# Optimization experiments

Measured on AMD Instinct MI355X. Metric: run time of the kernel, lower is better.

The kernel has to match this reference:

```python
import jax, jax.numpy as jnp
import numpy as np

G, H, D = 8, 16, 64           # groups, heads-per-group, head_size
B, S = 2, 1024                # sequences, tokens per sequence (T = B*S packed)
HID = G * H * D               # 8192
SCALE = D ** -0.5


def _rotary(x, cos, sin):
    # NeoX-style rotary. x: [T, nh, D]; cos/sin: [T, D//2]
    half = D // 2
    c = cos[:, None, :]
    s = sin[:, None, :]
    x1, x2 = x[..., :half], x[..., half:]
    return jnp.concatenate([x1 * c - x2 * s, x2 * c + x1 * s], axis=-1)


def setup_inputs() -> dict:
    key = jax.random.key(0)
    ks = jax.random.split(key, 6)
    T = B * S
    hidden_states = jax.random.normal(ks[0], (T, HID), jnp.float32)
    # true rotary tables from positions (base 10000)
    pos = jnp.tile(jnp.arange(S, dtype=jnp.float32), B)            # [T]
    inv_freq = 1.0 / (10000.0 ** (jnp.arange(0, D, 2, dtype=jnp.float32) / D))
    freqs = pos[:, None] * inv_freq[None, :]                       # [T, D//2]
    cos, sin = jnp.cos(freqs), jnp.sin(freqs)
    w_qkv = jax.random.normal(ks[1], (HID, G * (H + 2) * D), jnp.float32) * (HID ** -0.5)
    b_qkv = jax.random.normal(ks[2], (G * (H + 2) * D,), jnp.float32) * 0.02
    w_dense = jax.random.normal(ks[3], (G * H * D, HID), jnp.float32) * (HID ** -0.5)
    b_dense = jax.random.normal(ks[4], (HID,), jnp.float32) * 0.02
    kv_cache = jnp.zeros((2, 4096, G, D), jnp.float32)
    slots = jnp.arange(T, dtype=jnp.int32)
    return dict(hidden_states=hidden_states, cos=cos, sin=sin,
                w_qkv=w_qkv, b_qkv=b_qkv, w_dense=w_dense, b_dense=b_dense,
                kv_cache=kv_cache, slots=slots, batch_size=B)


def reference(hidden_states, cos, sin, w_qkv, b_qkv, w_dense, b_dense,
              kv_cache, slots, batch_size):
    T = hidden_states.shape[0]
    qkv = hidden_states @ w_qkv + b_qkv                    # [T, G*(H+2)*D]
    qkv = qkv.reshape(T, G, H + 2, D)
    query = qkv[:, :, :H, :].reshape(T, G * H, D)          # [T, G*H, D]
    k = qkv[:, :, H, :]                                    # [T, G, D]
    v = qkv[:, :, H + 1, :]                                # [T, G, D]

    query = _rotary(query, cos, sin)
    k = _rotary(k, cos, sin)

    # reshape_and_cache: write rotated K and V into the slot cache
    new_cache = kv_cache.at[0, slots].set(k).at[1, slots].set(v)

    # prefill flash attention, causal, GQA (each group's K/V shared by H heads)
    q = query.reshape(batch_size, S, G, H, D)
    kb = k.reshape(batch_size, S, G, D)
    vb = v.reshape(batch_size, S, G, D)
    scores = jnp.einsum('bsghd,btgd->bghst', q, kb) * SCALE  # [B,G,H,S,S]
    causal = jnp.tril(jnp.ones((S, S), bool))
    scores = jnp.where(causal, scores, jnp.finfo(scores.dtype).min)
    probs = jax.nn.softmax(scores, axis=-1)
    attn = jnp.einsum('bghst,btgd->bsghd', probs, vb)        # [B,S,G,H,D]
    attn = attn.reshape(T, G * H * D)
    out = attn @ w_dense + b_dense                           # [T, HID]
    return out, new_cache
```

## Files before the change

kernel.cpp:

```cpp
#include <hip/hip_runtime.h>

#define T_TOK 2048
#define HIDD  8192
#define NQKV  9216
#define GG    8
#define HH    16
#define DD    64
#define SS    1024
#define BB    2
#define SCALE_ATTN 0.125f

typedef __attribute__((ext_vector_type(4))) float f32x4;
typedef __attribute__((ext_vector_type(8))) short bf16x8;

#define GLOBAL_AS __attribute__((address_space(1)))
#define LDS_AS    __attribute__((address_space(3)))

__device__ __forceinline__ void glds16(const void* g, void* l) {
  __builtin_amdgcn_global_load_lds((GLOBAL_AS void*)(g), (LDS_AS void*)(l), 16, 0, 0);
}

__device__ __forceinline__ ushort f2bf(float f) {
  union { float f; unsigned u; } v; v.f = f;
  unsigned u = v.u + 0x7fffu + ((v.u >> 16) & 1u);
  return (ushort)(u >> 16);
}

__global__ void cvt_bf16_kernel(const float* __restrict__ in, ushort* __restrict__ out, int n4) {
  int i = blockIdx.x * 256 + threadIdx.x;
  if (i >= n4) return;
  float4 v = ((const float4*)in)[i];
  ushort4 o;
  o.x = f2bf(v.x); o.y = f2bf(v.y); o.z = f2bf(v.z); o.w = f2bf(v.w);
  ((ushort4*)out)[i] = o;
}

__global__ void copy_f32_kernel(const float* __restrict__ in, float* __restrict__ out, int n4) {
  int i = blockIdx.x * 256 + threadIdx.x;
  if (i < n4) ((float4*)out)[i] = ((const float4*)in)[i];
}

__global__ __launch_bounds__(256) void transpose_bf16_kernel(
    const float* __restrict__ in, ushort* __restrict__ out, int R, int C)
{
  __shared__ float tile[64][65];
  const int c0 = blockIdx.x * 64, r0 = blockIdx.y * 64;
  const int tid = threadIdx.x;
  const int tx = tid & 15, iy = tid >> 4;
  #pragma unroll
  for (int p = 0; p < 4; ++p) {
    const int i = iy + p * 16;
    const float4 v = *(const float4*)&in[(size_t)(r0 + i) * C + c0 + tx * 4];
    tile[i][tx * 4 + 0] = v.x; tile[i][tx * 4 + 1] = v.y;
    tile[i][tx * 4 + 2] = v.z; tile[i][tx * 4 + 3] = v.w;
  }
  __syncthreads();
  const int r4 = tid & 15, cg = tid >> 4;
  #pragma unroll
  for (int p = 0; p < 4; ++p) {
    const int c = cg + p * 16;
    ushort4 o;
    o.x = f2bf(tile[r4 * 4 + 0][c]);
    o.y = f2bf(tile[r4 * 4 + 1][c]);
    o.z = f2bf(tile[r4 * 4 + 2][c]);
    o.w = f2bf(tile[r4 * 4 + 3][c]);
    *(ushort4*)&out[(size_t)(c0 + c) * R + r0 + r4 * 4] = o;
  }
}

__global__ __launch_bounds__(256, 2) void gemm_bt_kernel(
    const ushort* __restrict__ A, const ushort* __restrict__ Bt,
    const float* __restrict__ bias, float* __restrict__ C,
    int M, int N, int K)
{
  __shared__ __align__(16) ushort As[128 * 32];
  __shared__ __align__(16) ushort Bs[128 * 32];
  const int tid = threadIdx.x;
  const int wid = tid >> 6, lane = tid & 63;
  const int kg = lane >> 4, ln = lane & 15;
  const int m0 = blockIdx.y * 128, n0 = blockIdx.x * 128;
  const int wm = (wid >> 1) * 64, wn = (wid & 1) * 64;

  f32x4 acc[4][4] = {};

  const int e_base = wid * 1024;
  const int e0 = e_base + lane * 8;
  const int e1 = e_base + 512 + lane * 8;
  const int r0a = e0 >> 5, c0a = e0 & 31;
  const int r1a = e1 >> 5, c1a = e1 & 31;

  const ushort* Ap0 = A + (size_t)(m0 + r0a) * K + c0a;
  const ushort* Ap1 = A + (size_t)(m0 + r1a) * K + c1a;
  const ushort* Bp0 = Bt + (size_t)(n0 + r0a) * K + c0a;
  const ushort* Bp1 = Bt + (size_t)(n0 + r1a) * K + c1a;
  ushort* lA0 = &As[e_base];
  ushort* lA1 = &As[e_base + 512];
  ushort* lB0 = &Bs[e_base];
  ushort* lB1 = &Bs[e_base + 512];

  for (int k0 = 0; k0 < K; k0 += 32) {
    glds16(Ap0 + k0, lA0);
    glds16(Ap1 + k0, lA1);
    glds16(Bp0 + k0, lB0);
    glds16(Bp1 + k0, lB1);
    __syncthreads();
    bf16x8 af[4], bfr[4];
    #pragma unroll
    for (int t = 0; t < 4; ++t) {
      af[t]  = *(const bf16x8*)&As[(wm + t * 16 + ln) * 32 + kg * 8];
      bfr[t] = *(const bf16x8*)&Bs[(wn + t * 16 + ln) * 32 + kg * 8];
    }
    #pragma unroll
    for (int i = 0; i < 4; ++i)
      #pragma unroll
      for (int j = 0; j < 4; ++j)
        acc[i][j] = __builtin_amdgcn_mfma_f32_16x16x32_bf16(af[i], bfr[j], acc[i][j], 0, 0, 0);
    __syncthreads();
  }

  #pragma unroll
  for (int i = 0; i < 4; ++i) {
    const int row = m0 + wm + i * 16 + kg * 4;
    #pragma unroll
    for (int j = 0; j < 4; ++j) {
      const int col = n0 + wn + j * 16 + ln;
      const float bv = bias[col];
      #pragma unroll
      for (int r = 0; r < 4; ++r)
        C[(size_t)(row + r) * N + col] = acc[i][j][r] + bv;
    }
  }
}

__global__ void rotary_scatter_kernel(const float* __restrict__ qkv,
                                      const float* __restrict__ cosb, const float* __restrict__ sinb,
                                      const int* __restrict__ slots,
                                      ushort* __restrict__ Qr, ushort* __restrict__ Kr,
                                      ushort* __restrict__ Vr, float* __restrict__ cache)
{
  const int t = blockIdx.x;
  const int b = t >> 10, s = t & 1023;
  const int slot = slots[t];
  for (int j = threadIdx.x; j < GG * 18 * 32; j += 256) {
    const int g = j / 576;
    const int rem = j - g * 576;
    const int head = rem >> 5;
    const int d = rem & 31;
    const float* row = qkv + (size_t)t * NQKV + g * 1152 + head * 64;
    const float x1 = row[d], x2 = row[d + 32];
    const float c = cosb[t * 32 + d], s_ = sinb[t * 32 + d];
    if (head < 16) {
      const size_t o = ((size_t)((b * 128 + g * 16 + head) * 1024 + s)) * 64;
      Qr[o + d]      = f2bf(x1 * c - x2 * s_);
      Qr[o + 32 + d] = f2bf(x2 * c + x1 * s_);
    } else if (head == 16) {
      const float o1 = x1 * c - x2 * s_, o2 = x2 * c + x1 * s_;
      const size_t o = ((size_t)((b * 8 + g) * 1024 + s)) * 64;
      Kr[o + d] = f2bf(o1); Kr[o + 32 + d] = f2bf(o2);
      const size_t co = ((size_t)slot * GG + g) * 64;
      cache[co + d] = o1; cache[co + 32 + d] = o2;
    } else {
      const size_t vo = ((size_t)((b * 8 + g) * 64 + d)) * 1024 + s;
      Vr[vo] = f2bf(x1);
      Vr[vo + (size_t)32 * 1024] = f2bf(x2);
      const size_t co = (size_t)4096 * GG * 64 + ((size_t)slot * GG + g) * 64;
      cache[co + d] = x1; cache[co + 32 + d] = x2;
    }
  }
}

__global__ __launch_bounds__(256, 4) void flash_attn_kernel(
    const ushort* __restrict__ Q, const ushort* __restrict__ Kc,
    const ushort* __restrict__ Vc, ushort* __restrict__ O)
{
  const int qb = blockIdx.x;
  const int gh = blockIdx.y;
  const int g  = gh >> 4;
  const int b  = blockIdx.z;
  const int tid = threadIdx.x;
  const int wid = tid >> 6, lane = tid & 63;
  const int kg = lane >> 4, ln = lane & 15;

  __shared__ __align__(16) ushort Ks[64 * 72];
  __shared__ __align__(16) ushort Vt[64 * 72];
  __shared__ __align__(16) ushort Ps[128 * 72];

  bf16x8 qf[2][2];
  #pragma unroll
  for (int st = 0; st < 2; ++st) {
    const int sq = qb * 128 + wid * 32 + st * 16 + ln;
    const size_t qoff = ((size_t)((b * 128 + gh) * 1024 + sq)) * 64;
    qf[st][0] = *(const bf16x8*)&Q[qoff + kg * 8];
    qf[st][1] = *(const bf16x8*)&Q[qoff + 32 + kg * 8];
  }

  f32x4 acc_o[2][4] = {};
  float m_i[2][4], l_i[2][4];
  #pragma unroll
  for (int st = 0; st < 2; ++st)
    #pragma unroll
    for (int r = 0; r < 4; ++r) { m_i[st][r] = -1e30f; l_i[st][r] = 0.f; }

  const size_t kbase = ((size_t)(b * 8 + g) * 1024) * 64;
  const size_t vbase = ((size_t)(b * 8 + g) * 64) * 1024;

  const int n_it = 2 * qb + 2;
  for (int it = 0; it < n_it; ++it) {
    const int t0 = it * 64;
    __syncthreads();
    #pragma unroll
    for (int rep = 0; rep < 2; ++rep) {
      const int idx = rep * 256 + tid;
      const int rr = idx >> 3, c8 = (idx & 7) * 8;
      *(uint4*)&Ks[rr * 72 + c8] = *(const uint4*)&Kc[kbase + (size_t)(t0 + rr) * 64 + c8];
      *(uint4*)&Vt[rr * 72 + c8] = *(const uint4*)&Vc[vbase + (size_t)rr * 1024 + t0 + c8];
    }
    __syncthreads();

    f32x4 sc[2][4];
    #pragma unroll
    for (int tt = 0; tt < 4; ++tt) {
      const bf16x8 kf0 = *(const bf16x8*)&Ks[(tt * 16 + ln) * 72 + kg * 8];
      const bf16x8 kf1 = *(const bf16x8*)&Ks[(tt * 16 + ln) * 72 + 32 + kg * 8];
      #pragma unroll
      for (int st = 0; st < 2; ++st) {
        f32x4 z = {};
        z = __builtin_amdgcn_mfma_f32_16x16x32_bf16(qf[st][0], kf0, z, 0, 0, 0);
        z = __builtin_amdgcn_mfma_f32_16x16x32_bf16(qf[st][1], kf1, z, 0, 0, 0);
        sc[st][tt] = z;
      }
    }

    if (it >= 2 * qb) {
      #pragma unroll
      for (int st = 0; st < 2; ++st) {
        const int srow = qb * 128 + wid * 32 + st * 16 + kg * 4;
        #pragma unroll
        for (int tt = 0; tt < 4; ++tt) {
          const int tg = t0 + tt * 16 + ln;
          #pragma unroll
          for (int r = 0; r < 4; ++r)
            sc[st][tt][r] = (tg <= srow + r) ? sc[st][tt][r] * SCALE_ATTN : -1e30f;
        }
      }
    } else {
      #pragma unroll
      for (int st = 0; st < 2; ++st)
        #pragma unroll
        for (int tt = 0; tt < 4; ++tt)
          #pragma unroll
          for (int r = 0; r < 4; ++r)
            sc[st][tt][r] *= SCALE_ATTN;
    }

    #pragma unroll
    for (int st = 0; st < 2; ++st) {
      float alpha[4];
      #pragma unroll
      for (int r = 0; r < 4; ++r) {
        float mx = fmaxf(fmaxf(sc[st][0][r], sc[st][1][r]), fmaxf(sc[st][2][r], sc[st][3][r]));
        #pragma unroll
        for (int off = 1; off < 16; off <<= 1)
          mx = fmaxf(mx, __shfl_xor(mx, off, 64));
        const float mn = fmaxf(m_i[st][r], mx);
        float rs = 0.f;
        #pragma unroll
        for (int tt = 0; tt < 4; ++tt) {
          const float p = __expf(sc[st][tt][r] - mn);
          sc[st][tt][r] = p; rs += p;
        }
        #pragma unroll
        for (int off = 1; off < 16; off <<= 1)
          rs += __shfl_xor(rs, off, 64);
        alpha[r] = __expf(m_i[st][r] - mn);
        l_i[st][r] = l_i[st][r] * alpha[r] + rs;
        m_i[st][r] = mn;
      }
      #pragma unroll
      for (int dt = 0; dt < 4; ++dt)
        #pragma unroll
        for (int r = 0; r < 4; ++r)
          acc_o[st][dt][r] *= alpha[r];
      #pragma unroll
      for (int tt = 0; tt < 4; ++tt)
        #pragma unroll
        for (int r = 0; r < 4; ++r)
          Ps[(wid * 32 + st * 16 + kg * 4 + r) * 72 + tt * 16 + ln] = f2bf(sc[st][tt][r]);
    }
    __syncthreads();

    #pragma unroll
    for (int c = 0; c < 2; ++c) {
      bf16x8 vf[4];
      #pragma unroll
      for (int dt = 0; dt < 4; ++dt)
        vf[dt] = *(const bf16x8*)&Vt[(dt * 16 + ln) * 72 + c * 32 + kg * 8];
      #pragma unroll
      for (int st = 0; st < 2; ++st) {
        const bf16x8 pf = *(const bf16x8*)&Ps[(wid * 32 + st * 16 + ln) * 72 + c * 32 + kg * 8];
        #pragma unroll
        for (int dt = 0; dt < 4; ++dt)
          acc_o[st][dt] = __builtin_amdgcn_mfma_f32_16x16x32_bf16(pf, vf[dt], acc_o[st][dt], 0, 0, 0);
      }
    }
  }

  #pragma unroll
  for (int st = 0; st < 2; ++st) {
    const int srow = qb * 128 + wid * 32 + st * 16 + kg * 4;
    #pragma unroll
    for (int dt = 0; dt < 4; ++dt) {
      #pragma unroll
      for (int r = 0; r < 4; ++r) {
        const float o = acc_o[st][dt][r] / l_i[st][r];
        O[((size_t)(b * 1024 + srow + r)) * 8192 + gh * 64 + dt * 16 + ln] = f2bf(o);
      }
    }
  }
}

#define WS0_HB   ((size_t)0)
#define WS1_WT   ((size_t)33554432)
#define WS2_QKV  ((size_t)(33554432 + 150994944))
#define WS3_QR   (WS2_QKV + (size_t)75497472)
#define WS4_KR   (WS3_QR + (size_t)33554432)
#define WS5_VR   (WS4_KR + (size_t)2097152)

extern "C" void kernel_launch(void* const* d_in, const int* in_sizes, int n_in,
                              void* d_out, int out_size, void* d_ws, size_t ws_size,
                              hipStream_t stream) {
  const float* hidden  = (const float*)d_in[0];
  const float* cosb    = (const float*)d_in[1];
  const float* sinb    = (const float*)d_in[2];
  const float* w_qkv   = (const float*)d_in[3];
  const float* b_qkv   = (const float*)d_in[4];
  const float* w_dense = (const float*)d_in[5];
  const float* b_dense = (const float*)d_in[6];
  const float* kv_in   = (const float*)d_in[7];
  const int*   slots   = (const int*)d_in[8];

  float* out = (float*)d_out;
  float* out_cache = out + (size_t)T_TOK * HIDD;

  char* ws = (char*)d_ws;
  ushort* hb   = (ushort*)(ws + WS0_HB);
  ushort* wT   = (ushort*)(ws + WS1_WT);
  float*  qkv  = (float*)(ws + WS2_QKV);
  ushort* qr   = (ushort*)(ws + WS3_QR);
  ushort* kr   = (ushort*)(ws + WS4_KR);
  ushort* vr   = (ushort*)(ws + WS5_VR);
  ushort* attn = hb;

  cvt_bf16_kernel<<<(T_TOK * HIDD / 4 + 255) / 256, 256, 0, stream>>>(hidden, hb, T_TOK * HIDD / 4);
  transpose_bf16_kernel<<<dim3(NQKV / 64, HIDD / 64), 256, 0, stream>>>(w_qkv, wT, HIDD, NQKV);
  gemm_bt_kernel<<<dim3(NQKV / 128, T_TOK / 128), 256, 0, stream>>>(hb, wT, b_qkv, qkv, T_TOK, NQKV, HIDD);
  copy_f32_kernel<<<(2 * 4096 * GG * DD / 4 + 255) / 256, 256, 0, stream>>>(kv_in, out_cache, 2 * 4096 * GG * DD / 4);
  rotary_scatter_kernel<<<T_TOK, 256, 0, stream>>>(qkv, cosb, sinb, slots, qr, kr, vr, out_cache);
  transpose_bf16_kernel<<<dim3(HIDD / 64, HIDD / 64), 256, 0, stream>>>(w_dense, wT, HIDD, HIDD);
  flash_attn_kernel<<<dim3(SS / 128, GG * HH, BB), 256, 0, stream>>>(qr, kr, vr, attn);
  gemm_bt_kernel<<<dim3(HIDD / 128, T_TOK / 128), 256, 0, stream>>>(attn, wT, b_dense, out, T_TOK, HIDD, HIDD);
}
```

Before: 1.793 ms.

## Rewrite bf16 GEMM with 256x256 tiles, 4-stage LDS pipeline, and block swizzle

The GEMM now uses 512-thread blocks computing 256x256 output tiles, with each wave holding a 128x64 sub-tile. A four-deep ring of LDS buffers is filled by async global-to-LDS loads issued three k-steps ahead, gated by vmcnt waits and a single barrier per step. A block-index swizzle is added for L2 locality, and s_setprio raises wave priority around the MFMA bursts. The aim is to hide global-load latency and cut per-FLOP load traffic. The cost is 128 KB of LDS per block and heavy register use, which will likely limit occupancy to one block per CU. The swizzle assumes the block count is divisible by 8.

```diff
diff --git a/kernel.cpp b/kernel.cpp
--- a/kernel.cpp
+++ b/kernel.cpp
@@ -68,66 +68,101 @@
   }
 }
 
-__global__ __launch_bounds__(256, 2) void gemm_bt_kernel(
+__global__ __launch_bounds__(512, 2) void gemm_bt_kernel(
     const ushort* __restrict__ A, const ushort* __restrict__ Bt,
     const float* __restrict__ bias, float* __restrict__ C,
     int M, int N, int K)
 {
-  __shared__ __align__(16) ushort As[128 * 32];
-  __shared__ __align__(16) ushort Bs[128 * 32];
+  __shared__ __align__(16) ushort lds[4 * 16384];
   const int tid = threadIdx.x;
   const int wid = tid >> 6, lane = tid & 63;
   const int kg = lane >> 4, ln = lane & 15;
-  const int m0 = blockIdx.y * 128, n0 = blockIdx.x * 128;
-  const int wm = (wid >> 1) * 64, wn = (wid & 1) * 64;
-
-  f32x4 acc[4][4] = {};
-
-  const int e_base = wid * 1024;
-  const int e0 = e_base + lane * 8;
-  const int e1 = e_base + 512 + lane * 8;
-  const int r0a = e0 >> 5, c0a = e0 & 31;
-  const int r1a = e1 >> 5, c1a = e1 & 31;
-
-  const ushort* Ap0 = A + (size_t)(m0 + r0a) * K + c0a;
-  const ushort* Ap1 = A + (size_t)(m0 + r1a) * K + c1a;
-  const ushort* Bp0 = Bt + (size_t)(n0 + r0a) * K + c0a;
-  const ushort* Bp1 = Bt + (size_t)(n0 + r1a) * K + c1a;
-  ushort* lA0 = &As[e_base];
-  ushort* lA1 = &As[e_base + 512];
-  ushort* lB0 = &Bs[e_base];
-  ushort* lB1 = &Bs[e_base + 512];
-
-  for (int k0 = 0; k0 < K; k0 += 32) {
-    glds16(Ap0 + k0, lA0);
-    glds16(Ap1 + k0, lA1);
-    glds16(Bp0 + k0, lB0);
-    glds16(Bp1 + k0, lB1);
-    __syncthreads();
-    bf16x8 af[4], bfr[4];
-    #pragma unroll
-    for (int t = 0; t < 4; ++t) {
-      af[t]  = *(const bf16x8*)&As[(wm + t * 16 + ln) * 32 + kg * 8];
-      bfr[t] = *(const bf16x8*)&Bs[(wn + t * 16 + ln) * 32 + kg * 8];
-    }
-    #pragma unroll
-    for (int i = 0; i < 4; ++i)
-      #pragma unroll
-      for (int j = 0; j < 4; ++j)
-        acc[i][j] = __builtin_amdgcn_mfma_f32_16x16x32_bf16(af[i], bfr[j], acc[i][j], 0, 0, 0);
-    __syncthreads();
-  }
-
-  #pragma unroll
-  for (int i = 0; i < 4; ++i) {
-    const int row = m0 + wm + i * 16 + kg * 4;
-    #pragma unroll
-    for (int j = 0; j < 4; ++j) {
-      const int col = n0 + wn + j * 16 + ln;
-      const float bv = bias[col];
+
+  const int nwg = gridDim.x * gridDim.y;
+  const int lin = blockIdx.y * gridDim.x + blockIdx.x;
+  const int swz = (lin & 7) * (nwg >> 3) + (lin >> 3);
+  const int bx = swz % gridDim.x, by = swz / gridDim.x;
+
+  const int m0 = by * 256, n0 = bx * 256;
+  const int wm = (wid >> 2) << 7;
+  const int wn = (wid & 3) << 6;
+
+  f32x4 acc[8][4] = {};
+
+  const int r0 = tid >> 2, sl = (tid & 3) * 8;
+  const ushort* Ap0 = A  + (size_t)(m0 + r0) * K + sl;
+  const ushort* Ap1 = A  + (size_t)(m0 + r0 + 128) * K + sl;
+  const ushort* Bp0 = Bt + (size_t)(n0 + r0) * K + sl;
+  const ushort* Bp1 = Bt + (size_t)(n0 + r0 + 128) * K + sl;
+  ushort* wbA = lds + wid * 512;
+  ushort* wbB = lds + 8192 + wid * 512;
+
+  const int NT = K >> 5;
+
+#define STAGE(t) {                                        \
+    const int kk = (t) * 32;                              \
+    const int bo = ((t) & 3) * 16384;                     \
+    glds16(Ap0 + kk, wbA + bo);                           \
+    glds16(Ap1 + kk, wbA + bo + 4096);                    \
+    glds16(Bp0 + kk, wbB + bo);                           \
+    glds16(Bp1 + kk, wbB + bo + 4096);                    \
+  }
+
+#define COMPUTE(t) {                                                          \
+    const ushort* bufA = lds + ((t) & 3) * 16384;                             \
+    const ushort* bufB = bufA + 8192;                                         \
+    bf16x8 af[8], bv[4];                                                      \
+    _Pragma("unroll")                                                         \
+    for (int mi = 0; mi < 8; ++mi)                                            \
+      af[mi] = *(const bf16x8*)&bufA[(wm + mi * 16 + ln) * 32 + kg * 8];      \
+    _Pragma("unroll")                                                         \
+    for (int ni = 0; ni < 4; ++ni)                                            \
+      bv[ni] = *(const bf16x8*)&bufB[(wn + ni * 16 + ln) * 32 + kg * 8];      \
+    __builtin_amdgcn_s_setprio(1);                                            \
+    _Pragma("unroll")                                                         \
+    for (int mi = 0; mi < 8; ++mi)                                            \
+      _Pragma("unroll")                                                       \
+      for (int ni = 0; ni < 4; ++ni)                                          \
+        acc[mi][ni] = __builtin_amdgcn_mfma_f32_16x16x32_bf16(                \
+            af[mi], bv[ni], acc[mi][ni], 0, 0, 0);                            \
+    __builtin_amdgcn_s_setprio(0);                                            \
+  }
+
+  STAGE(0); STAGE(1); STAGE(2);
+
+  for (int t = 0; t < NT - 3; ++t) {
+    asm volatile("s_waitcnt vmcnt(8)" ::: "memory");
+    __builtin_amdgcn_s_barrier();
+    asm volatile("" ::: "memory");
+    STAGE(t + 3);
+    COMPUTE(t);
+  }
+  asm volatile("s_waitcnt vmcnt(8)" ::: "memory");
+  __builtin_amdgcn_s_barrier();
+  asm volatile("" ::: "memory");
+  COMPUTE(NT - 3);
+  asm volatile("s_waitcnt vmcnt(4)" ::: "memory");
+  __builtin_amdgcn_s_barrier();
+  asm volatile("" ::: "memory");
+  COMPUTE(NT - 2);
+  asm volatile("s_waitcnt vmcnt(0)" ::: "memory");
+  __builtin_amdgcn_s_barrier();
+  asm volatile("" ::: "memory");
+  COMPUTE(NT - 1);
+
+#undef STAGE
+#undef COMPUTE
+
+  #pragma unroll
+  for (int mi = 0; mi < 8; ++mi) {
+    const int row = m0 + wm + mi * 16 + kg * 4;
+    #pragma unroll
+    for (int ni = 0; ni < 4; ++ni) {
+      const int col = n0 + wn + ni * 16 + ln;
+      const float bvv = bias[col];
       #pragma unroll
       for (int r = 0; r < 4; ++r)
-        C[(size_t)(row + r) * N + col] = acc[i][j][r] + bv;
+        C[(size_t)(row + r) * N + col] = acc[mi][ni][r] + bvv;
     }
   }
 }
@@ -353,10 +388,10 @@
 
   cvt_bf16_kernel<<<(T_TOK * HIDD / 4 + 255) / 256, 256, 0, stream>>>(hidden, hb, T_TOK * HIDD / 4);
   transpose_bf16_kernel<<<dim3(NQKV / 64, HIDD / 64), 256, 0, stream>>>(w_qkv, wT, HIDD, NQKV);
-  gemm_bt_kernel<<<dim3(NQKV / 128, T_TOK / 128), 256, 0, stream>>>(hb, wT, b_qkv, qkv, T_TOK, NQKV, HIDD);
+  gemm_bt_kernel<<<dim3(NQKV / 256, T_TOK / 256), 512, 0, stream>>>(hb, wT, b_qkv, qkv, T_TOK, NQKV, HIDD);
   copy_f32_kernel<<<(2 * 4096 * GG * DD / 4 + 255) / 256, 256, 0, stream>>>(kv_in, out_cache, 2 * 4096 * GG * DD / 4);
   rotary_scatter_kernel<<<T_TOK, 256, 0, stream>>>(qkv, cosb, sinb, slots, qr, kr, vr, out_cache);
   transpose_bf16_kernel<<<dim3(HIDD / 64, HIDD / 64), 256, 0, stream>>>(w_dense, wT, HIDD, HIDD);
   flash_attn_kernel<<<dim3(SS / 128, GG * HH, BB), 256, 0, stream>>>(qr, kr, vr, attn);
-  gemm_bt_kernel<<<dim3(HIDD / 128, T_TOK / 128), 256, 0, stream>>>(attn, wT, b_dense, out, T_TOK, HIDD, HIDD);
-}
+  gemm_bt_kernel<<<dim3(HIDD / 256, T_TOK / 256), 512, 0, stream>>>(attn, wT, b_dense, out, T_TOK, HIDD, HIDD);
+}
```

Result: no change. 1.794 ms (+0.0%).
